# Kernel optimization log

Measured on AMD Instinct MI355X. Metric: run time of the kernel, lower is better.

The kernel has to match this reference:

```python
import jax, jax.numpy as jnp
import numpy as np

HID = 128
NUM_HEADS = 8
NUM_LAYERS = 3
N_OP, N_MA, N_JOB = 50000, 1000, 5000
E_SIZES = [150000, 100000, 150000, 100000, 100000]
# (src_type, dst_type) for the 5 edge relations, in module order:
# precedence, assigned_to, can_process, contains, belongs_to
EDGE_SD = [("operation", "operation"), ("operation", "machine"), ("machine", "operation"), ("job", "operation"), ("operation", "job")]
NT_IDX = {"operation": 0, "machine": 1, "job": 2}


def setup_inputs() -> dict:
    key = jax.random.key(0)
    ks = list(jax.random.split(key, 80))
    it = iter(ks)

    def nrm(shape, scale=1.0):
        return jax.random.normal(next(it), shape, dtype=jnp.float32) * scale

    n_nodes = {"operation": N_OP, "machine": N_MA, "job": N_JOB}
    inp = {}
    inp["x_operation"] = nrm((N_OP, 64))
    inp["x_machine"] = nrm((N_MA, 32))
    inp["x_job"] = nrm((N_JOB, 16))
    ei_names = ["ei_prec", "ei_assign", "ei_canproc", "ei_contains", "ei_belongs"]
    ea_names = ["ea_prec", "ea_assign", "ea_canproc", "ea_contains", "ea_belongs"]
    for ne, na, E, (st, dt) in zip(ei_names, ea_names, E_SIZES, EDGE_SD):
        src = jax.random.randint(next(it), (E,), 0, n_nodes[st], dtype=jnp.int32)
        dst = jax.random.randint(next(it), (E,), 0, n_nodes[dt], dtype=jnp.int32)
        inp[ne] = jnp.stack([src, dst])
        inp[na] = nrm((E, 32))
    # node input projections (per-type dims)
    inp["Wn_op"] = nrm((64, HID), 64 ** -0.5)
    inp["bn_op"] = jnp.zeros((HID,), jnp.float32)
    inp["Wn_ma"] = nrm((32, HID), 32 ** -0.5)
    inp["bn_ma"] = jnp.zeros((HID,), jnp.float32)
    inp["Wn_job"] = nrm((16, HID), 16 ** -0.5)
    inp["bn_job"] = jnp.zeros((HID,), jnp.float32)
    # edge attr projections: 5 relations, 32 -> HID, applied once before the layers
    inp["We_proj"] = nrm((5, 32, HID), 32 ** -0.5)
    inp["be_proj"] = jnp.zeros((5, HID), jnp.float32)
    # GATConv params stacked as [layer, edge_type, ...]; heads*out == HID at every layer
    inp["Wg"] = nrm((NUM_LAYERS, 5, HID, HID), HID ** -0.5)      # shared lin for src/dst
    inp["att_s"] = nrm((NUM_LAYERS, 5, HID), HID ** -0.5)
    inp["att_d"] = nrm((NUM_LAYERS, 5, HID), HID ** -0.5)
    inp["Wge"] = nrm((NUM_LAYERS, 5, HID, HID), HID ** -0.5)     # lin_edge
    inp["att_e"] = nrm((NUM_LAYERS, 5, HID), HID ** -0.5)
    inp["bg"] = jnp.zeros((NUM_LAYERS, 5, HID), jnp.float32)      # GATConv output bias
    # BatchNorm affine: [layer, node_type, HID]
    inp["gamma"] = jnp.ones((NUM_LAYERS, 3, HID), jnp.float32)
    inp["beta"] = jnp.zeros((NUM_LAYERS, 3, HID), jnp.float32)
    # output projection for 'operation'
    inp["Wo"] = nrm((HID, HID), HID ** -0.5)
    inp["bo"] = jnp.zeros((HID,), jnp.float32)
    return inp


def _segment_softmax(logits, seg, num):
    # PyG softmax: exp(x - segment_max) / (segment_sum + 1e-16)
    m = jax.ops.segment_max(logits, seg, num_segments=num)
    m = jnp.where(jnp.isfinite(m), m, 0.0)  # empty segments -> 0
    ex = jnp.exp(logits - m[seg])
    den = jax.ops.segment_sum(ex, seg, num_segments=num)
    return ex / (den[seg] + 1e-16)


def _gat_forward(x_operation, x_machine, x_job, eis, eas_raw,
                 Wn_op, bn_op, Wn_ma, bn_ma, Wn_job, bn_job,
                 We_proj, be_proj, Wg, att_s, att_d, Wge, att_e, bg,
                 gamma, beta, Wo, bo):
    x = {
        "operation": x_operation @ Wn_op + bn_op,
        "machine": x_machine @ Wn_ma + bn_ma,
        "job": x_job @ Wn_job + bn_job,
    }
    # edge attrs projected once to HID
    eas = [eas_raw[t] @ We_proj[t] + be_proj[t] for t in range(5)]

    for i in range(NUM_LAYERS):
        H = NUM_HEADS if i < NUM_LAYERS - 1 else 1
        C = HID // H
        resid = x
        agg = {nt: jnp.zeros((x[nt].shape[0], HID), x[nt].dtype) for nt in x}
        for t, (st, dt) in enumerate(EDGE_SD):
            src, dst = eis[t][0], eis[t][1]
            n_dst = x[dt].shape[0]
            xs = (x[st] @ Wg[i, t]).reshape(-1, H, C)            # [Ns,H,C]
            xd = (x[dt] @ Wg[i, t]).reshape(-1, H, C)            # [Nd,H,C]
            a_s = (xs * att_s[i, t].reshape(H, C)).sum(-1)       # [Ns,H]
            a_d = (xd * att_d[i, t].reshape(H, C)).sum(-1)       # [Nd,H]
            e = (eas[t] @ Wge[i, t]).reshape(-1, H, C)           # [E,H,C]
            a_e = (e * att_e[i, t].reshape(H, C)).sum(-1)        # [E,H]
            logits = jax.nn.leaky_relu(a_s[src] + a_d[dst] + a_e, 0.2)
            alpha = _segment_softmax(logits, dst, n_dst)         # [E,H]
            msg = xs[src] * alpha[:, :, None]                    # [E,H,C]
            out = jax.ops.segment_sum(msg, dst, num_segments=n_dst)
            agg[dt] = agg[dt] + out.reshape(n_dst, HID) + bg[i, t]
        new_x = {}
        for nt in x:
            h = agg[nt]
            mu = h.mean(0)
            var = ((h - mu) ** 2).mean(0)  # biased, as BatchNorm1d training
            h = (h - mu) * jax.lax.rsqrt(var + 1e-5) * gamma[i, NT_IDX[nt]] + beta[i, NT_IDX[nt]]
            if i < NUM_LAYERS - 1:
                h = jax.nn.relu(h)  # dropout is identity in eval
            new_x[nt] = h + resid[nt]  # residual (dims always match: HID)
        x = new_x
    return x["operation"] @ Wo + bo


def reference(x_operation, x_machine, x_job,
              ei_prec, ei_assign, ei_canproc, ei_contains, ei_belongs,
              ea_prec, ea_assign, ea_canproc, ea_contains, ea_belongs,
              Wn_op, bn_op, Wn_ma, bn_ma, Wn_job, bn_job,
              We_proj, be_proj, Wg, att_s, att_d, Wge, att_e, bg,
              gamma, beta, Wo, bo):
    eis = [ei_prec, ei_assign, ei_canproc, ei_contains, ei_belongs]
    eas = [ea_prec, ea_assign, ea_canproc, ea_contains, ea_belongs]
    return _gat_forward(x_operation, x_machine, x_job, eis, eas,
                        Wn_op, bn_op, Wn_ma, bn_ma, Wn_job, bn_job,
                        We_proj, be_proj, Wg, att_s, att_d, Wge, att_e, bg,
                        gamma, beta, Wo, bo)
```

## Files before the change

### kernel.cpp

```cpp
#include <hip/hip_runtime.h>
#include <cstdint>

#define HID 128

static constexpr int kNOp = 50000, kNMa = 1000, kNJob = 5000;
static constexpr int kNTot = 56000;
static constexpr int kETot = 600000;
static constexpr int kSeg = 156000;
static constexpr int kEsz[5]   = {150000, 100000, 150000, 100000, 100000};
static constexpr int kSrcT[5]  = {0, 0, 1, 2, 0};
static constexpr int kDstT[5]  = {0, 1, 0, 0, 2};
static constexpr int kNodeOff[3] = {0, 50000, 51000};
static constexpr int kSoff[5]  = {0, 0, 50000, 51000, 0};
static constexpr int kDoff[5]  = {0, 50000, 0, 0, 51000};
static constexpr int kEoff[6]  = {0, 150000, 250000, 400000, 500000, 600000};
static constexpr int kRoff[5]  = {0, 50000, 100000, 101000, 106000};
static constexpr int kRTot = 156000;

typedef __attribute__((ext_vector_type(8))) __bf16 bf16x8;
typedef __attribute__((ext_vector_type(4))) float f32x4;

__device__ inline unsigned short f2b(float f) {
  unsigned u = __float_as_uint(f);
  unsigned r = (u + 0x7FFFu + ((u >> 16) & 1u)) >> 16;
  return (unsigned short)r;
}
__device__ inline float b2f(unsigned short u) {
  return __uint_as_float(((unsigned)u) << 16);
}

__device__ inline int seg_of(int t, int d) {
  if (t == 0) return 3 * d;
  if (t == 2) return 3 * d + 1;
  if (t == 3) return 3 * d + 2;
  if (t == 1) return 150000 + d;
  return 151000 + d;
}

__global__ void conv_pad(const float* __restrict__ in, unsigned short* __restrict__ out,
                         int M, int K, int Kp) {
  int i = blockIdx.x * blockDim.x + threadIdx.x;
  if (i >= M * Kp) return;
  int r = i / Kp, c = i - r * Kp;
  out[i] = (c < K) ? f2b(in[(size_t)r * K + c]) : (unsigned short)0;
}

__global__ void transpose_w(const float* __restrict__ W, unsigned short* __restrict__ Wt,
                            int K, int N, int Kp, int nmat) {
  int i = blockIdx.x * blockDim.x + threadIdx.x;
  int per = N * Kp;
  if (i >= nmat * per) return;
  int b = i / per, rem = i - b * per;
  int n = rem / Kp, k = rem - n * Kp;
  Wt[i] = (k < K) ? f2b(W[(size_t)b * K * N + (size_t)k * N + n]) : (unsigned short)0;
}

template <int KC>
__global__ __launch_bounds__(256) void gemm_mfma(
    const unsigned short* __restrict__ A, const unsigned short* __restrict__ Bt,
    const float* __restrict__ bias, float* __restrict__ Cf,
    unsigned short* __restrict__ Cb, int M) {
  const int K = KC * 32;
  int w = blockIdx.x * 4 + (threadIdx.x >> 6);
  int m0 = w * 16;
  if (m0 >= M) return;
  int lane = threadIdx.x & 63;
  int l16 = lane & 15, quad = lane >> 4;
  int xrow = m0 + l16; if (xrow >= M) xrow = M - 1;
  bf16x8 xf[KC];
#pragma unroll
  for (int kc = 0; kc < KC; kc++) {
    int4 raw = *(const int4*)(A + (size_t)xrow * K + kc * 32 + quad * 8);
    xf[kc] = __builtin_bit_cast(bf16x8, raw);
  }
  bool wr = (m0 + l16 < M);
  int row = m0 + l16;
#pragma unroll
  for (int nt = 0; nt < 8; nt++) {
    f32x4 acc = {0.f, 0.f, 0.f, 0.f};
#pragma unroll
    for (int kc = 0; kc < KC; kc++) {
      int4 braw = *(const int4*)(Bt + (size_t)(nt * 16 + l16) * K + kc * 32 + quad * 8);
      acc = __builtin_amdgcn_mfma_f32_16x16x32_bf16(
          __builtin_bit_cast(bf16x8, braw), xf[kc], acc, 0, 0, 0);
    }
    int col0 = nt * 16 + quad * 4;
    float o[4];
#pragma unroll
    for (int r = 0; r < 4; r++) o[r] = acc[r] + (bias ? bias[col0 + r] : 0.f);
    if (wr) {
      if (Cf) *(float4*)(Cf + (size_t)row * HID + col0) = make_float4(o[0], o[1], o[2], o[3]);
      if (Cb) *(ushort4*)(Cb + (size_t)row * HID + col0) =
                  make_ushort4(f2b(o[0]), f2b(o[1]), f2b(o[2]), f2b(o[3]));
    }
  }
}

__global__ __launch_bounds__(256) void gemm_xs(const unsigned short* __restrict__ x,
                                               const unsigned short* __restrict__ WgTl,
                                               unsigned short* __restrict__ xs) {
  __shared__ __align__(16) unsigned short Bs[128 * 136];
  __shared__ __align__(16) unsigned short Os[4][16 * 136];
  int b = blockIdx.x;
  int grp = (b < 782) ? 0 : (b < 798 ? 1 : 2);
  int sb   = (grp == 0) ? 0     : (grp == 1 ? 782   : 798);
  int M    = (grp == 0) ? 50000 : (grp == 1 ? 1000  : 5000);
  int xoff = (grp == 0) ? 0     : (grp == 1 ? 50000 : 51000);
  int tid = threadIdx.x;
  int wid = tid >> 6, lane = tid & 63;
  int l16 = lane & 15, quad = lane >> 4;
  int m0 = (b - sb) * 64 + wid * 16;
  int xrow = m0 + l16; if (xrow >= M) xrow = M - 1;
  bf16x8 xf[4];
#pragma unroll
  for (int kc = 0; kc < 4; kc++) {
    int4 raw = *(const int4*)(x + (size_t)(xoff + xrow) * HID + kc * 32 + quad * 8);
    xf[kc] = __builtin_bit_cast(bf16x8, raw);
  }
  int nrel = (grp == 0) ? 3 : 1;
  int rel0  = (grp == 0) ? 0 : (grp == 1 ? 2 : 3);
  int roff0 = (grp == 0) ? 0 : (grp == 1 ? 100000 : 101000);
  int rels[3]  = {rel0, 1, 4};
  int roffs[3] = {roff0, 50000, 106000};
  for (int rr = 0; rr < nrel; rr++) {
    int t = rels[rr];
    unsigned short* Cb = xs + (size_t)roffs[rr] * HID;
    __syncthreads();
    const unsigned short* Wsrc = WgTl + (size_t)t * HID * HID;
    for (int c = tid; c < 2048; c += 256) {
      int row = c >> 4, k8 = c & 15;
      *(int4*)&Bs[row * 136 + k8 * 8] = *(const int4*)(Wsrc + row * 128 + k8 * 8);
    }
    __syncthreads();
#pragma unroll
    for (int nt = 0; nt < 8; nt++) {
      f32x4 acc = {0.f, 0.f, 0.f, 0.f};
#pragma unroll
      for (int kc = 0; kc < 4; kc++) {
        bf16x8 bfr = *(const bf16x8*)&Bs[(nt * 16 + l16) * 136 + kc * 32 + quad * 8];
        acc = __builtin_amdgcn_mfma_f32_16x16x32_bf16(bfr, xf[kc], acc, 0, 0, 0);
      }
      *(ushort4*)&Os[wid][l16 * 136 + nt * 16 + quad * 4] =
          make_ushort4(f2b(acc[0]), f2b(acc[1]), f2b(acc[2]), f2b(acc[3]));
    }
#pragma unroll
    for (int i = 0; i < 4; i++) {
      int g = i * 1024 + lane * 16;
      int row = g >> 8;
      int colb = g & 255;
      int4 v = *(const int4*)((const char*)&Os[wid][0] + row * 272 + colb);
      if (m0 + row < M)
        *(int4*)((char*)(Cb + (size_t)(m0 + row) * HID) + colb) = v;
    }
  }
}

template <int NCOL>
__global__ __launch_bounds__(256) void gemm_as(
    const unsigned short* __restrict__ A, const unsigned short* __restrict__ Bt,
    float* __restrict__ out, int M) {
  int w = blockIdx.x * 4 + (threadIdx.x >> 6);
  int m0 = w * 16;
  if (m0 >= M) return;
  int lane = threadIdx.x & 63;
  int l16 = lane & 15, quad = lane >> 4;
  int xrow = m0 + l16; if (xrow >= M) xrow = M - 1;
  bf16x8 xf[4];
#pragma unroll
  for (int kc = 0; kc < 4; kc++) {
    int4 raw = *(const int4*)(A + (size_t)xrow * HID + kc * 32 + quad * 8);
    xf[kc] = __builtin_bit_cast(bf16x8, raw);
  }
  bool wr = (m0 + l16 < M);
  int row = m0 + l16;
#pragma unroll
  for (int nt = 0; nt < NCOL / 16; nt++) {
    f32x4 acc = {0.f, 0.f, 0.f, 0.f};
#pragma unroll
    for (int kc = 0; kc < 4; kc++) {
      int4 braw = *(const int4*)(Bt + (size_t)(nt * 16 + l16) * HID + kc * 32 + quad * 8);
      acc = __builtin_amdgcn_mfma_f32_16x16x32_bf16(
          __builtin_bit_cast(bf16x8, braw), xf[kc], acc, 0, 0, 0);
    }
    if (wr) {
      int col0 = nt * 16 + quad * 4;
      *(float4*)(out + (size_t)row * NCOL + col0) = make_float4(acc[0], acc[1], acc[2], acc[3]);
    }
  }
}

__global__ void fold_kernel(const float* __restrict__ Wg, const float* __restrict__ att_s,
                            const float* __restrict__ att_d, const float* __restrict__ Wge,
                            const float* __restrict__ att_e, const float* __restrict__ Wep,
                            const float* __restrict__ bep,
                            float* __restrict__ S, float* __restrict__ D,
                            float* __restrict__ w32, float* __restrict__ cvec) {
  int idx = blockIdx.x;
  int h = idx & 7, lt = idx >> 3;
  int l = lt / 5;
  int H = (l < 2) ? 8 : 1, C = HID / H;
  if (h >= H) return;
  int k = threadIdx.x;
  int t = lt % 5;
  const float* wg  = Wg  + (size_t)lt * HID * HID;
  const float* wge = Wge + (size_t)lt * HID * HID;
  const float* as_ = att_s + (size_t)lt * HID + h * C;
  const float* ad_ = att_d + (size_t)lt * HID + h * C;
  const float* ae_ = att_e + (size_t)lt * HID + h * C;
  float s = 0.f, d = 0.f, v = 0.f;
  for (int c = 0; c < C; c++) {
    float wr = wg[(size_t)k * HID + h * C + c];
    s += wr * as_[c];
    d += wr * ad_[c];
    v += wge[(size_t)k * HID + h * C + c] * ae_[c];
  }
  S[(size_t)idx * HID + k] = s;
  D[(size_t)idx * HID + k] = d;
  __shared__ float vs[HID];
  vs[k] = v;
  __syncthreads();
  if (k < 32) {
    const float* wp = Wep + (size_t)t * 32 * HID + (size_t)k * HID;
    float a = 0.f;
    for (int j = 0; j < HID; j++) a += wp[j] * vs[j];
    w32[(size_t)idx * 32 + k] = a;
  }
  if (k == 32) {
    const float* bp = bep + (size_t)t * HID;
    float a = 0.f;
    for (int j = 0; j < HID; j++) a += bp[j] * vs[j];
    cvec[idx] = a;
  }
}

__global__ void build_vb(const float* __restrict__ Sv, const float* __restrict__ Dv,
                         unsigned short* __restrict__ VbT) {
  int i = blockIdx.x * 256 + threadIdx.x;
  if (i >= 3 * 80 * HID) return;
  int l = i / (80 * HID), rem = i % (80 * HID);
  int col = rem / HID, k = rem % HID;
  int H = (l < 2) ? 8 : 1;
  float val = 0.f;
  if (col < 10 * H) {
    int v = col / H, h = col % H;
    const float* base = (v < 5) ? Sv : Dv;
    int t = (v < 5) ? v : v - 5;
    val = base[((size_t)(l * 5 + t) * 8 + h) * HID + k];
  }
  VbT[i] = f2b(val);
}

struct EdgeJobs {
  const int* src[5]; const int* dst[5];
};

__global__ void hist_rank(EdgeJobs J, int* __restrict__ cnt, int* __restrict__ rank) {
  int e = blockIdx.x * 256 + threadIdx.x;
  if (e >= kETot) return;
  int t = 0;
  while (t < 4 && e >= kEoff[t + 1]) t++;
  int d = J.dst[t][e - kEoff[t]];
  rank[e] = atomicAdd(&cnt[seg_of(t, d)], 1);
}

__global__ void scatter_b(EdgeJobs J, const int* __restrict__ rs,
                          const int* __restrict__ rank, int4* __restrict__ edat) {
  int e = blockIdx.x * 256 + threadIdx.x;
  if (e >= kETot) return;
  int t = 0;
  while (t < 4 && e >= kEoff[t + 1]) t++;
  int el = e - kEoff[t];
  int s = J.src[t][el];
  int d = J.dst[t][el];
  int p = rs[seg_of(t, d)] + rank[e];
  edat[p] = make_int4(e, ((s + kSoff[t]) << 3) | t, ((d + kDoff[t]) << 3) | t,
                      s + kRoff[t]);
}

__global__ void scan_blocks(const int* __restrict__ in, int* __restrict__ out,
                            int* __restrict__ bsums, int n) {
  __shared__ int sh[256];
  int t = threadIdx.x;
  int base = blockIdx.x * 1024 + t * 4;
  int v[4]; int s = 0;
#pragma unroll
  for (int j = 0; j < 4; j++) { v[j] = (base + j < n) ? in[base + j] : 0; s += v[j]; }
  sh[t] = s;
  __syncthreads();
  for (int off = 1; off < 256; off <<= 1) {
    int x = (t >= off) ? sh[t - off] : 0;
    __syncthreads();
    sh[t] += x;
    __syncthreads();
  }
  int run = sh[t] - s;
#pragma unroll
  for (int j = 0; j < 4; j++) { if (base + j < n) out[base + j] = run; run += v[j]; }
  if (t == 255) bsums[blockIdx.x] = sh[255];
}

__global__ void scan_carry(int* bsums, int nb, int* sentinel) {
  if (threadIdx.x == 0 && blockIdx.x == 0) {
    int run = 0;
    for (int b = 0; b < nb; b++) { int x = bsums[b]; bsums[b] = run; run += x; }
    *sentinel = run;
  }
}

__global__ void scan_add(int* __restrict__ out, const int* __restrict__ bsums, int n) {
  int base = blockIdx.x * 1024 + threadIdx.x * 4;
  int c = bsums[blockIdx.x];
#pragma unroll
  for (int j = 0; j < 4; j++) if (base + j < n) out[base + j] += c;
}

struct FoldAeJobs {
  const float* ea[5];
  int E[5]; int bpref[6];
};

__global__ __launch_bounds__(256) void fold_ae(FoldAeJobs J, const float* __restrict__ w32,
                                               const float* __restrict__ cv,
                                               float* __restrict__ aet0, float* __restrict__ aet1,
                                               float* __restrict__ aet2) {
  int b = blockIdx.x;
  int t = 0;
  while (t < 4 && b >= J.bpref[t + 1]) t++;
  __shared__ float w[3][8][32];
  __shared__ float cc[3][8];
  for (int i = threadIdx.x; i < 3 * 8 * 32; i += 256) {
    int l = i >> 8, rem = i & 255;
    w[l][rem >> 5][rem & 31] = w32[(size_t)((l * 5 + t) * 8) * 32 + rem];
  }
  if (threadIdx.x < 24) {
    int l = threadIdx.x >> 3, h = threadIdx.x & 7;
    cc[l][h] = cv[(size_t)(l * 5 + t) * 8 + h];
  }
  __syncthreads();
  int e = (b - J.bpref[t]) * 256 + threadIdx.x;
  if (e >= J.E[t]) return;
  int eg = kEoff[t] + e;
  float x[32];
  const float4* p4 = (const float4*)(J.ea[t] + (size_t)e * 32);
#pragma unroll
  for (int i = 0; i < 8; i++) {
    float4 v = p4[i];
    x[4 * i] = v.x; x[4 * i + 1] = v.y; x[4 * i + 2] = v.z; x[4 * i + 3] = v.w;
  }
  float o[8];
#pragma unroll
  for (int h = 0; h < 8; h++) {
    float a = cc[0][h];
#pragma unroll
    for (int k = 0; k < 32; k++) a += x[k] * w[0][h][k];
    o[h] = a;
  }
  float4* d0 = (float4*)(aet0 + (size_t)eg * 8);
  d0[0] = make_float4(o[0], o[1], o[2], o[3]);
  d0[1] = make_float4(o[4], o[5], o[6], o[7]);
#pragma unroll
  for (int h = 0; h < 8; h++) {
    float a = cc[1][h];
#pragma unroll
    for (int k = 0; k < 32; k++) a += x[k] * w[1][h][k];
    o[h] = a;
  }
  float4* d1 = (float4*)(aet1 + (size_t)eg * 8);
  d1[0] = make_float4(o[0], o[1], o[2], o[3]);
  d1[1] = make_float4(o[4], o[5], o[6], o[7]);
  float a = cc[2][0];
#pragma unroll
  for (int k = 0; k < 32; k++) a += x[k] * w[2][0][k];
  aet2[eg] = a;
}

__global__ __launch_bounds__(256) void pass_a8(const int4* __restrict__ edat,
                                               const float* __restrict__ aet,
                                               const float* __restrict__ AS,
                                               float* __restrict__ logits) {
  int p = blockIdx.x * 256 + threadIdx.x;
  if (p >= kETot) return;
  int4 ed = edat[p];
  int e = ed.x, sv = ed.y, dv = ed.z;
  int t = sv & 7;
  const float4* asp = (const float4*)(AS + (size_t)(sv >> 3) * 80 + t * 8);
  const float4* adp = (const float4*)(AS + (size_t)(dv >> 3) * 80 + (5 + t) * 8);
  const float4* aep = (const float4*)(aet + (size_t)e * 8);
  float4 s0 = asp[0], s1 = asp[1];
  float4 d0 = adp[0], d1 = adp[1];
  float4 e0 = aep[0], e1 = aep[1];
  float v[8] = {s0.x + d0.x + e0.x, s0.y + d0.y + e0.y, s0.z + d0.z + e0.z, s0.w + d0.w + e0.w,
                s1.x + d1.x + e1.x, s1.y + d1.y + e1.y, s1.z + d1.z + e1.z, s1.w + d1.w + e1.w};
#pragma unroll
  for (int j = 0; j < 8; j++) v[j] = v[j] > 0.f ? v[j] : 0.2f * v[j];
  float4* L = (float4*)(logits + (size_t)p * 8);
  L[0] = make_float4(v[0], v[1], v[2], v[3]);
  L[1] = make_float4(v[4], v[5], v[6], v[7]);
}

__global__ __launch_bounds__(256) void pass_a1(const int4* __restrict__ edat,
                                               const float* __restrict__ aet2,
                                               const float* __restrict__ AS,
                                               float* __restrict__ logits) {
  int p = blockIdx.x * 256 + threadIdx.x;
  if (p >= kETot) return;
  int4 ed = edat[p];
  int e = ed.x, sv = ed.y, dv = ed.z;
  int t = sv & 7;
  float v = aet2[e] + AS[(size_t)(sv >> 3) * 16 + t] + AS[(size_t)(dv >> 3) * 16 + 5 + t];
  v = v > 0.f ? v : 0.2f * v;
  logits[p] = v;
}

template <int H>
__global__ void softmax_k(const int* __restrict__ rs, float* __restrict__ lg) {
  int g = (int)((blockIdx.x * (size_t)blockDim.x + threadIdx.x) >> 6);
  int lane = threadIdx.x & 63;
  if (g >= kSeg) return;
  int start = rs[g], end = rs[g + 1];
  int n = (end - start) * H;
  if (n == 0) return;
  float* L = lg + (size_t)start * H;
  if (n <= 256) {
    float v[4];
#pragma unroll
    for (int j = 0; j < 4; j++) {
      int idx = lane + 64 * j;
      v[j] = (idx < n) ? L[idx] : -3.0e38f;
    }
    float m = fmaxf(fmaxf(v[0], v[1]), fmaxf(v[2], v[3]));
    if (H == 8) {
      m = fmaxf(m, __shfl_xor(m, 8));
      m = fmaxf(m, __shfl_xor(m, 16));
      m = fmaxf(m, __shfl_xor(m, 32));
    } else {
#pragma unroll
      for (int off = 1; off < 64; off <<= 1) m = fmaxf(m, __shfl_xor(m, off));
    }
    float s = 0.f;
#pragma unroll
    for (int j = 0; j < 4; j++) {
      v[j] = __expf(v[j] - m);
      s += v[j];
    }
    if (H == 8) {
      s += __shfl_xor(s, 8);
      s += __shfl_xor(s, 16);
      s += __shfl_xor(s, 32);
    } else {
#pragma unroll
      for (int off = 1; off < 64; off <<= 1) s += __shfl_xor(s, off);
    }
    float inv = 1.f / (s + 1e-16f);
#pragma unroll
    for (int j = 0; j < 4; j++) {
      int idx = lane + 64 * j;
      if (idx < n) L[idx] = v[j] * inv;
    }
    return;
  }
  float m = -3.0e38f;
  for (int idx = lane; idx < n; idx += 64) m = fmaxf(m, L[idx]);
  if (H == 8) {
    m = fmaxf(m, __shfl_xor(m, 8));
    m = fmaxf(m, __shfl_xor(m, 16));
    m = fmaxf(m, __shfl_xor(m, 32));
  } else {
#pragma unroll
    for (int off = 1; off < 64; off <<= 1) m = fmaxf(m, __shfl_xor(m, off));
  }
  float s = 0.f;
  for (int idx = lane; idx < n; idx += 64) {
    float ex = __expf(L[idx] - m);
    L[idx] = ex;
    s += ex;
  }
  if (H == 8) {
    s += __shfl_xor(s, 8);
    s += __shfl_xor(s, 16);
    s += __shfl_xor(s, 32);
  } else {
#pragma unroll
    for (int off = 1; off < 64; off <<= 1) s += __shfl_xor(s, off);
  }
  float inv = 1.f / (s + 1e-16f);
  for (int idx = lane; idx < n; idx += 64) L[idx] *= inv;
}

template <int H>
__global__ void gat_gather_u(const int* __restrict__ rs, const int4* __restrict__ edat,
                             const float* __restrict__ alpha,
                             const unsigned short* __restrict__ xs,
                             float* __restrict__ agg) {
  int g = (int)((blockIdx.x * (size_t)blockDim.x + threadIdx.x) >> 6);
  int lane = threadIdx.x & 63;
  if (g >= kNTot) return;
  int start, end;
  if (g < 50000)      { start = rs[3 * g];              end = rs[3 * g + 3]; }
  else if (g < 51000) { int m = g - 50000; start = rs[150000 + m]; end = rs[150001 + m]; }
  else                { int j = g - 51000; start = rs[151000 + j]; end = rs[151001 + j]; }
  int deg = end - start;
  int l16 = lane & 15, quad = lane >> 4;
  int h = (H == 8) ? (l16 >> 1) : 0;
  float acc[8] = {0.f, 0.f, 0.f, 0.f, 0.f, 0.f, 0.f, 0.f};
  for (int base = 0; base < deg; base += 64) {
    int nchunk = deg - base; if (nchunk > 64) nchunk = 64;
    int sv = (lane < nchunk) ? edat[start + base + lane].w : 0;
    for (int i = 0; i < nchunk; i += 4) {
      int e = i + quad;
      bool act = e < nchunk;
      int s = __shfl(sv, act ? e : 0);
      float w = act ? alpha[(size_t)(start + base + e) * H + h] : 0.f;
      int4 raw = *(const int4*)(xs + (size_t)s * HID + l16 * 8);
      unsigned ua[4] = {(unsigned)raw.x, (unsigned)raw.y, (unsigned)raw.z, (unsigned)raw.w};
#pragma unroll
      for (int j = 0; j < 4; j++) {
        acc[2 * j]     += w * __uint_as_float(ua[j] << 16);
        acc[2 * j + 1] += w * __uint_as_float(ua[j] & 0xFFFF0000u);
      }
    }
  }
#pragma unroll
  for (int j = 0; j < 8; j++) {
    acc[j] += __shfl_xor(acc[j], 16);
    acc[j] += __shfl_xor(acc[j], 32);
  }
  if (quad == 0) {
    float* p = agg + (size_t)g * HID + l16 * 8;
    *(float4*)p = make_float4(acc[0], acc[1], acc[2], acc[3]);
    *(float4*)(p + 4) = make_float4(acc[4], acc[5], acc[6], acc[7]);
  }
}

__global__ void colstats_b(const float* __restrict__ x, float* __restrict__ stats) {
  static constexpr int bpref[4] = {0, 384, 400, 448};
  static constexpr int rowoff[4] = {0, 50000, 51000, 56000};
  int b = blockIdx.x;
  int t = 0;
  while (t < 2 && b >= bpref[t + 1]) t++;
  int bl = b - bpref[t], nb = bpref[t + 1] - bpref[t];
  int tid = threadIdx.x;
  int col = tid & 127, half = tid >> 7;
  float s = 0.f, q = 0.f;
  for (int r = rowoff[t] + bl * 2 + half; r < rowoff[t + 1]; r += nb * 2) {
    float v = x[(size_t)r * HID + col];
    s += v; q += v * v;
  }
  __shared__ float ls[256], lq[256];
  ls[tid] = s; lq[tid] = q;
  __syncthreads();
  if (tid < 128) {
    s = ls[tid] + ls[tid + 128];
    q = lq[tid] + lq[tid + 128];
    unsafeAtomicAdd(&stats[t * 256 + col], s);
    unsafeAtomicAdd(&stats[t * 256 + 128 + col], q);
  }
}

__global__ void bn_apply_b(float* __restrict__ agg, const float* __restrict__ xold,
                           unsigned short* __restrict__ xnb, const float* __restrict__ stats,
                           const float* __restrict__ gammaL, const float* __restrict__ betaL,
                           int relu) {
  size_t i = blockIdx.x * (size_t)blockDim.x + threadIdx.x;
  if (i >= (size_t)kNTot * 32) return;
  int row = (int)(i >> 5);
  int t = (row < 50000) ? 0 : (row < 51000 ? 1 : 2);
  float invN = (t == 0) ? (1.f / 50000.f) : (t == 1 ? (1.f / 1000.f) : (1.f / 5000.f));
  const float* st = stats + t * 256;
  const float* gm = gammaL + t * HID;
  const float* bt = betaL + t * HID;
  int c4 = ((int)(i & 31)) * 4;
  float4 av = ((const float4*)agg)[i];
  float4 xv = ((const float4*)xold)[i];
  float a[4] = {av.x, av.y, av.z, av.w};
  float xo[4] = {xv.x, xv.y, xv.z, xv.w};
  float o[4];
#pragma unroll
  for (int j = 0; j < 4; j++) {
    int c = c4 + j;
    float mu = st[c] * invN;
    float var = st[128 + c] * invN - mu * mu;
    float g = gm[c] * rsqrtf(var + 1e-5f);
    float v = (a[j] - mu) * g + bt[c];
    if (relu) v = fmaxf(v, 0.f);
    o[j] = v + xo[j];
  }
  ((float4*)agg)[i] = make_float4(o[0], o[1], o[2], o[3]);
  ((ushort4*)xnb)[i] = make_ushort4(f2b(o[0]), f2b(o[1]), f2b(o[2]), f2b(o[3]));
}

extern "C" void kernel_launch(void* const* d_in, const int* in_sizes, int n_in,
                              void* d_out, int out_size, void* d_ws, size_t ws_size,
                              hipStream_t stream) {
  const float* x_in[3] = {(const float*)d_in[0], (const float*)d_in[1], (const float*)d_in[2]};
  const int* ei[5];
  const float* ea[5];
  for (int t = 0; t < 5; t++) {
    ei[t] = (const int*)d_in[3 + 2 * t];
    ea[t] = (const float*)d_in[4 + 2 * t];
  }
  const float* Wn[3]  = {(const float*)d_in[13], (const float*)d_in[15], (const float*)d_in[17]};
  const float* bnb[3] = {(const float*)d_in[14], (const float*)d_in[16], (const float*)d_in[18]};
  const float* Wep   = (const float*)d_in[19];
  const float* bep   = (const float*)d_in[20];
  const float* Wg    = (const float*)d_in[21];
  const float* att_s = (const float*)d_in[22];
  const float* att_d = (const float*)d_in[23];
  const float* Wge   = (const float*)d_in[24];
  const float* att_e = (const float*)d_in[25];
  const float* gamma = (const float*)d_in[27];
  const float* beta  = (const float*)d_in[28];
  const float* Wo    = (const float*)d_in[29];
  const float* bo    = (const float*)d_in[30];

  float* ws = (float*)d_ws;
  size_t off = 0;
  auto alloc = [&](size_t n) { size_t o = off; off += (n + 255) & ~(size_t)255; return o; };
  auto allocb = [&](size_t n) { return alloc((n + 1) / 2); };

  float* bufA = ws + alloc((size_t)kNTot * HID);
  float* bufB = ws + alloc((size_t)kNTot * HID);
  unsigned short* xcurb = (unsigned short*)(ws + allocb((size_t)kNTot * HID));
  unsigned short* xs_all = (unsigned short*)(ws + allocb((size_t)kRTot * HID));
  unsigned short* WgT  = (unsigned short*)(ws + allocb((size_t)15 * HID * HID));
  unsigned short* WoT  = (unsigned short*)(ws + allocb((size_t)HID * HID));
  unsigned short* WnT_op  = (unsigned short*)(ws + allocb((size_t)HID * 64));
  unsigned short* WnT_ma  = (unsigned short*)(ws + allocb((size_t)HID * 32));
  unsigned short* WnT_job = (unsigned short*)(ws + allocb((size_t)HID * 32));
  unsigned short* VbT  = (unsigned short*)(ws + allocb((size_t)3 * 80 * HID));
  float* Sv     = ws + alloc((size_t)15 * 8 * HID);
  float* Dv     = ws + alloc((size_t)15 * 8 * HID);
  float* w32    = ws + alloc((size_t)15 * 8 * 32);
  float* cv     = ws + alloc((size_t)15 * 8);
  float* stats  = ws + alloc((size_t)3 * 256);
  float* ASbuf  = ws + alloc((size_t)kNTot * 80);
  float* logits = ws + alloc((size_t)kETot * 8 + 64);
  int* rs_all   = (int*)(ws + alloc((size_t)kSeg + 8));
  int4* edat    = (int4*)(ws + alloc((size_t)kETot * 4));
  float* aet0   = ws + alloc((size_t)kETot * 8);
  float* aet1   = ws + alloc((size_t)kETot * 8);
  float* aet2   = ws + alloc((size_t)kETot);
  unsigned short* xinb_op  = xs_all;
  unsigned short* xinb_ma  = xs_all + 3200000;
  unsigned short* xinb_job = xs_all + 3232000;
  int* cnt    = (int*)logits;
  int* rank   = (int*)(logits + 156032);
  int* bsums  = (int*)(logits + 756288);
  (void)ws_size; (void)in_sizes; (void)n_in; (void)out_size;

  float* xcur = bufA;
  float* agg  = bufB;

  EdgeJobs EJ;
  for (int t = 0; t < 5; t++) { EJ.src[t] = ei[t]; EJ.dst[t] = ei[t] + kEsz[t]; }
  hipMemsetAsync(cnt, 0, (size_t)kSeg * 4, stream);
  hist_rank<<<(kETot + 255) / 256, 256, 0, stream>>>(EJ, cnt, rank);
  int nb = (kSeg + 1023) / 1024;
  scan_blocks<<<nb, 256, 0, stream>>>(cnt, rs_all, bsums, kSeg);
  scan_carry<<<1, 64, 0, stream>>>(bsums, nb, rs_all + kSeg);
  scan_add<<<nb, 256, 0, stream>>>(rs_all, bsums, kSeg);
  scatter_b<<<(kETot + 255) / 256, 256, 0, stream>>>(EJ, rs_all, rank, edat);

  conv_pad<<<(kNOp * 64 + 255) / 256, 256, 0, stream>>>(x_in[0], xinb_op, kNOp, 64, 64);
  conv_pad<<<(kNMa * 32 + 255) / 256, 256, 0, stream>>>(x_in[1], xinb_ma, kNMa, 32, 32);
  conv_pad<<<(kNJob * 32 + 255) / 256, 256, 0, stream>>>(x_in[2], xinb_job, kNJob, 16, 32);
  transpose_w<<<(HID * 64 + 255) / 256, 256, 0, stream>>>(Wn[0], WnT_op, 64, HID, 64, 1);
  transpose_w<<<(HID * 32 + 255) / 256, 256, 0, stream>>>(Wn[1], WnT_ma, 32, HID, 32, 1);
  transpose_w<<<(HID * 32 + 255) / 256, 256, 0, stream>>>(Wn[2], WnT_job, 16, HID, 32, 1);
  transpose_w<<<(15 * HID * HID + 255) / 256, 256, 0, stream>>>(Wg, WgT, HID, HID, HID, 15);
  transpose_w<<<(HID * HID + 255) / 256, 256, 0, stream>>>(Wo, WoT, HID, HID, HID, 1);
  fold_kernel<<<120, 128, 0, stream>>>(Wg, att_s, att_d, Wge, att_e, Wep, bep,
                                       Sv, Dv, w32, cv);
  build_vb<<<(3 * 80 * HID + 255) / 256, 256, 0, stream>>>(Sv, Dv, VbT);

  static constexpr int foldBpref[6]  = {0, 587, 978, 1565, 1956, 2347};

  FoldAeJobs FJ;
  for (int t = 0; t < 5; t++) {
    FJ.ea[t] = ea[t];
    FJ.E[t] = kEsz[t];
    FJ.bpref[t] = foldBpref[t];
  }
  FJ.bpref[5] = foldBpref[5];
  fold_ae<<<foldBpref[5], 256, 0, stream>>>(FJ, w32, cv, aet0, aet1, aet2);

  gemm_mfma<2><<<((kNOp + 15) / 16 + 3) / 4, 256, 0, stream>>>(
      xinb_op, WnT_op, bnb[0], xcur, xcurb, kNOp);
  gemm_mfma<1><<<((kNMa + 15) / 16 + 3) / 4, 256, 0, stream>>>(
      xinb_ma, WnT_ma, bnb[1], xcur + (size_t)50000 * HID, xcurb + (size_t)50000 * HID, kNMa);
  gemm_mfma<1><<<((kNJob + 15) / 16 + 3) / 4, 256, 0, stream>>>(
      xinb_job, WnT_job, bnb[2], xcur + (size_t)51000 * HID, xcurb + (size_t)51000 * HID, kNJob);

  for (int l = 0; l < 3; l++) {
    int H = (l < 2) ? 8 : 1;

    gemm_xs<<<877, 256, 0, stream>>>(xcurb, WgT + (size_t)l * 5 * HID * HID, xs_all);

    int asBlocks = ((kNTot + 15) / 16 + 3) / 4;
    if (H == 8)
      gemm_as<80><<<asBlocks, 256, 0, stream>>>(xcurb, VbT + (size_t)l * 80 * HID, ASbuf, kNTot);
    else
      gemm_as<16><<<asBlocks, 256, 0, stream>>>(xcurb, VbT + (size_t)l * 80 * HID, ASbuf, kNTot);

    int pblocks = (kETot + 255) / 256;
    if (H == 8) {
      const float* aeL = (l == 0) ? aet0 : aet1;
      pass_a8<<<pblocks, 256, 0, stream>>>(edat, aeL, ASbuf, logits);
    } else {
      pass_a1<<<pblocks, 256, 0, stream>>>(edat, aet2, ASbuf, logits);
    }

    if (H == 8) {
      softmax_k<8><<<((size_t)kSeg * 64 + 255) / 256, 256, 0, stream>>>(rs_all, logits);
      gat_gather_u<8><<<((size_t)kNTot * 64 + 255) / 256, 256, 0, stream>>>(
          rs_all, edat, logits, xs_all, agg);
    } else {
      softmax_k<1><<<((size_t)kSeg * 64 + 255) / 256, 256, 0, stream>>>(rs_all, logits);
      gat_gather_u<1><<<((size_t)kNTot * 64 + 255) / 256, 256, 0, stream>>>(
          rs_all, edat, logits, xs_all, agg);
    }

    hipMemsetAsync(stats, 0, 3 * 256 * 4, stream);
    colstats_b<<<448, 256, 0, stream>>>(agg, stats);
    bn_apply_b<<<(unsigned)(((size_t)kNTot * 32 + 255) / 256), 256, 0, stream>>>(
        agg, xcur, xcurb, stats, gamma + (size_t)l * 3 * HID, beta + (size_t)l * 3 * HID,
        (l < 2) ? 1 : 0);
    float* tmp = xcur; xcur = agg; agg = tmp;
  }

  gemm_mfma<4><<<((kNOp + 15) / 16 + 3) / 4, 256, 0, stream>>>(
      xcurb, WoT, bo, (float*)d_out, nullptr, kNOp);
}
```

Baseline: 860.9 us.

## Compute edge-attention fold with split-bf16 MFMA instead of scalar FMAs

The per-edge projection of 32-dim edge attributes onto 17 attention columns now runs on matrix cores. Each wavefront handles 16 edges. Inputs and weights are split into hi/lo bf16 pairs and three MFMAs per output tile recover near-fp32 accuracy. A small setup kernel prepares the split weight matrices and biases. This replaces the scalar 544-FMA loop per thread at the cost of an extra launch and some precision loss from dropping the lo×lo term.

```diff
diff --git a/kernel.cpp b/kernel.cpp
--- a/kernel.cpp
+++ b/kernel.cpp
@@ -250,6 +250,23 @@
   VbT[i] = f2b(val);
 }
 
+__global__ void build_wf(const float* __restrict__ w32, const float* __restrict__ cv,
+                         unsigned short* __restrict__ Wfh, unsigned short* __restrict__ Wfl,
+                         float* __restrict__ ccv) {
+  int i = blockIdx.x * 256 + threadIdx.x;
+  if (i >= 5 * 32 * 32) return;
+  int t = i >> 10, rem = i & 1023;
+  int col = rem >> 5, k = rem & 31;
+  float val = 0.f, c = 0.f;
+  if (col < 8)        { val = w32[((size_t)((0 * 5 + t) * 8 + col)) * 32 + k];       c = cv[(0 * 5 + t) * 8 + col]; }
+  else if (col < 16)  { val = w32[((size_t)((1 * 5 + t) * 8 + (col - 8))) * 32 + k]; c = cv[(1 * 5 + t) * 8 + col - 8]; }
+  else if (col == 16) { val = w32[((size_t)((2 * 5 + t) * 8 + 0)) * 32 + k];         c = cv[(2 * 5 + t) * 8]; }
+  unsigned short h = f2b(val);
+  Wfh[i] = h;
+  Wfl[i] = f2b(val - b2f(h));
+  if (k == 0) ccv[t * 32 + col] = c;
+}
+
 struct EdgeJobs {
   const int* src[5]; const int* dst[5];
 };
@@ -316,62 +333,60 @@
 
 struct FoldAeJobs {
   const float* ea[5];
-  int E[5]; int bpref[6];
 };
 
-__global__ __launch_bounds__(256) void fold_ae(FoldAeJobs J, const float* __restrict__ w32,
-                                               const float* __restrict__ cv,
+__global__ __launch_bounds__(256) void fold_ae(FoldAeJobs J,
+                                               const unsigned short* __restrict__ Wfh,
+                                               const unsigned short* __restrict__ Wfl,
+                                               const float* __restrict__ ccv,
                                                float* __restrict__ aet0, float* __restrict__ aet1,
                                                float* __restrict__ aet2) {
-  int b = blockIdx.x;
+  int w = blockIdx.x * 4 + (threadIdx.x >> 6);
+  int eg0 = w * 16;
+  if (eg0 >= kETot) return;
   int t = 0;
-  while (t < 4 && b >= J.bpref[t + 1]) t++;
-  __shared__ float w[3][8][32];
-  __shared__ float cc[3][8];
-  for (int i = threadIdx.x; i < 3 * 8 * 32; i += 256) {
-    int l = i >> 8, rem = i & 255;
-    w[l][rem >> 5][rem & 31] = w32[(size_t)((l * 5 + t) * 8) * 32 + rem];
-  }
-  if (threadIdx.x < 24) {
-    int l = threadIdx.x >> 3, h = threadIdx.x & 7;
-    cc[l][h] = cv[(size_t)(l * 5 + t) * 8 + h];
-  }
-  __syncthreads();
-  int e = (b - J.bpref[t]) * 256 + threadIdx.x;
-  if (e >= J.E[t]) return;
-  int eg = kEoff[t] + e;
-  float x[32];
-  const float4* p4 = (const float4*)(J.ea[t] + (size_t)e * 32);
+  while (t < 4 && eg0 >= kEoff[t + 1]) t++;
+  int lane = threadIdx.x & 63;
+  int l16 = lane & 15, quad = lane >> 4;
+  int el = eg0 - kEoff[t] + l16;
+  const float4* p4 = (const float4*)(J.ea[t] + (size_t)el * 32 + quad * 8);
+  float4 a = p4[0], b = p4[1];
+  float xv[8] = {a.x, a.y, a.z, a.w, b.x, b.y, b.z, b.w};
+  unsigned hi[8], lo[8];
 #pragma unroll
   for (int i = 0; i < 8; i++) {
-    float4 v = p4[i];
-    x[4 * i] = v.x; x[4 * i + 1] = v.y; x[4 * i + 2] = v.z; x[4 * i + 3] = v.w;
-  }
-  float o[8];
-#pragma unroll
-  for (int h = 0; h < 8; h++) {
-    float a = cc[0][h];
-#pragma unroll
-    for (int k = 0; k < 32; k++) a += x[k] * w[0][h][k];
-    o[h] = a;
-  }
-  float4* d0 = (float4*)(aet0 + (size_t)eg * 8);
-  d0[0] = make_float4(o[0], o[1], o[2], o[3]);
-  d0[1] = make_float4(o[4], o[5], o[6], o[7]);
-#pragma unroll
-  for (int h = 0; h < 8; h++) {
-    float a = cc[1][h];
-#pragma unroll
-    for (int k = 0; k < 32; k++) a += x[k] * w[1][h][k];
-    o[h] = a;
-  }
-  float4* d1 = (float4*)(aet1 + (size_t)eg * 8);
-  d1[0] = make_float4(o[0], o[1], o[2], o[3]);
-  d1[1] = make_float4(o[4], o[5], o[6], o[7]);
-  float a = cc[2][0];
-#pragma unroll
-  for (int k = 0; k < 32; k++) a += x[k] * w[2][0][k];
-  aet2[eg] = a;
+    unsigned short h = f2b(xv[i]);
+    hi[i] = h;
+    lo[i] = f2b(xv[i] - b2f(h));
+  }
+  int4 hraw = make_int4((int)(hi[0] | (hi[1] << 16)), (int)(hi[2] | (hi[3] << 16)),
+                        (int)(hi[4] | (hi[5] << 16)), (int)(hi[6] | (hi[7] << 16)));
+  int4 lraw = make_int4((int)(lo[0] | (lo[1] << 16)), (int)(lo[2] | (lo[3] << 16)),
+                        (int)(lo[4] | (lo[5] << 16)), (int)(lo[6] | (lo[7] << 16)));
+  bf16x8 Ah = __builtin_bit_cast(bf16x8, hraw);
+  bf16x8 Al = __builtin_bit_cast(bf16x8, lraw);
+  size_t wb = (size_t)t * 1024 + (size_t)l16 * 32 + quad * 8;
+  bf16x8 B0h = __builtin_bit_cast(bf16x8, *(const int4*)(Wfh + wb));
+  bf16x8 B0l = __builtin_bit_cast(bf16x8, *(const int4*)(Wfl + wb));
+  bf16x8 B1h = __builtin_bit_cast(bf16x8, *(const int4*)(Wfh + wb + 512));
+  bf16x8 B1l = __builtin_bit_cast(bf16x8, *(const int4*)(Wfl + wb + 512));
+  float4 c0 = *(const float4*)(ccv + t * 32 + quad * 4);
+  float4 c1 = *(const float4*)(ccv + t * 32 + 16 + quad * 4);
+  f32x4 acc0 = {c0.x, c0.y, c0.z, c0.w};
+  f32x4 acc1 = {c1.x, c1.y, c1.z, c1.w};
+  acc0 = __builtin_amdgcn_mfma_f32_16x16x32_bf16(B0h, Ah, acc0, 0, 0, 0);
+  acc0 = __builtin_amdgcn_mfma_f32_16x16x32_bf16(B0l, Ah, acc0, 0, 0, 0);
+  acc0 = __builtin_amdgcn_mfma_f32_16x16x32_bf16(B0h, Al, acc0, 0, 0, 0);
+  acc1 = __builtin_amdgcn_mfma_f32_16x16x32_bf16(B1h, Ah, acc1, 0, 0, 0);
+  acc1 = __builtin_amdgcn_mfma_f32_16x16x32_bf16(B1l, Ah, acc1, 0, 0, 0);
+  acc1 = __builtin_amdgcn_mfma_f32_16x16x32_bf16(B1h, Al, acc1, 0, 0, 0);
+  int eg = eg0 + l16;
+  float4 o = make_float4(acc0[0], acc0[1], acc0[2], acc0[3]);
+  if (quad == 0)      *(float4*)(aet0 + (size_t)eg * 8)     = o;
+  else if (quad == 1) *(float4*)(aet0 + (size_t)eg * 8 + 4) = o;
+  else if (quad == 2) *(float4*)(aet1 + (size_t)eg * 8)     = o;
+  else                *(float4*)(aet1 + (size_t)eg * 8 + 4) = o;
+  if (quad == 0) aet2[eg] = acc1[0];
 }
 
 __global__ __launch_bounds__(256) void pass_a8(const int4* __restrict__ edat,
@@ -628,6 +643,9 @@
   unsigned short* WnT_ma  = (unsigned short*)(ws + allocb((size_t)HID * 32));
   unsigned short* WnT_job = (unsigned short*)(ws + allocb((size_t)HID * 32));
   unsigned short* VbT  = (unsigned short*)(ws + allocb((size_t)3 * 80 * HID));
+  unsigned short* Wfh  = (unsigned short*)(ws + allocb((size_t)5 * 32 * 32));
+  unsigned short* Wfl  = (unsigned short*)(ws + allocb((size_t)5 * 32 * 32));
+  float* ccv    = ws + alloc((size_t)5 * 32);
   float* Sv     = ws + alloc((size_t)15 * 8 * HID);
   float* Dv     = ws + alloc((size_t)15 * 8 * HID);
   float* w32    = ws + alloc((size_t)15 * 8 * 32);
@@ -672,17 +690,11 @@
   fold_kernel<<<120, 128, 0, stream>>>(Wg, att_s, att_d, Wge, att_e, Wep, bep,
                                        Sv, Dv, w32, cv);
   build_vb<<<(3 * 80 * HID + 255) / 256, 256, 0, stream>>>(Sv, Dv, VbT);
-
-  static constexpr int foldBpref[6]  = {0, 587, 978, 1565, 1956, 2347};
+  build_wf<<<(5 * 32 * 32 + 255) / 256, 256, 0, stream>>>(w32, cv, Wfh, Wfl, ccv);
 
   FoldAeJobs FJ;
-  for (int t = 0; t < 5; t++) {
-    FJ.ea[t] = ea[t];
-    FJ.E[t] = kEsz[t];
-    FJ.bpref[t] = foldBpref[t];
-  }
-  FJ.bpref[5] = foldBpref[5];
-  fold_ae<<<foldBpref[5], 256, 0, stream>>>(FJ, w32, cv, aet0, aet1, aet2);
+  for (int t = 0; t < 5; t++) FJ.ea[t] = ea[t];
+  fold_ae<<<kETot / 64, 256, 0, stream>>>(FJ, Wfh, Wfl, ccv, aet0, aet1, aet2);
 
   gemm_mfma<2><<<((kNOp + 15) / 16 + 3) / 4, 256, 0, stream>>>(
       xinb_op, WnT_op, bnb[0], xcur, xcurb, kNOp);
```

After: 856.7 us. No clear change (-0.5%).
